# Optimization experiments

Measured on AMD Instinct MI355X. Metric: run time of the kernel, lower is better.

## Reference

```python
import jax, jax.numpy as jnp
import numpy as np

# ---- quantization scales (per-tensor, as produced by from_float calibration) ----
IN_SCALE = 0.05      # ForwardTokenizer: fp32 hidden -> int8
ALPHA_Q = 1e-4       # W8A8B8O8 requant multipliers (already include 1/sqrt(head_dim) for q)
ALPHA_K = 1e-4
ALPHA_V = 1e-4
QK_ALPHA = 1e-3      # BMM_S8T_S8N_F32T dequant scale (q_scale * k_scale)
PV_ALPHA = 1.0/127.0 # BMM_S8T_S8N_S8T requant scale ((1/127)*v_scale/out_scale)
OUT_ALPHA = 1e-4     # W8A8BFP32OFP32 dequant scale
NUM_HEADS = 32


def _quant_i8(x, scale):
    # simulate int8 quantization in fp32 (values are exact small integers)
    return jnp.clip(jnp.round(x / scale), -128.0, 127.0)


def _w8a8b8o8(x_i8, W_i8, b_i8, alpha):
    # int8 GEMM with int8 bias, requantized to int8: clamp(round(alpha*(x@W^T) + b))
    acc = jnp.einsum('btd,ed->bte', x_i8, W_i8)  # int32 accumulator in fp32
    return jnp.clip(jnp.round(alpha * acc + b_i8), -128.0, 127.0)


def setup_inputs() -> dict:
    key = jax.random.key(0)
    ks = jax.random.split(key, 10)
    B, T, D = 2, 2048, 2560
    hidden_states = jax.random.normal(ks[0], (B, T, D), dtype=jnp.float32)
    # causal additive mask, shape (B,1,T,T)
    neg = jnp.float32(-1e9)
    causal = jnp.where(jnp.tril(jnp.ones((T, T), dtype=bool)), 0.0, neg)
    attention_mask = jnp.broadcast_to(causal[None, None], (B, 1, T, T)).astype(jnp.float32)
    # int8-valued weights/biases stored as fp32 integers in [-127,127]
    def i8(k, shape):
        return jax.random.randint(k, shape, -127, 128).astype(jnp.float32)
    Wq = i8(ks[1], (D, D)); bq = i8(ks[2], (D,))
    Wk = i8(ks[3], (D, D)); bk = i8(ks[4], (D,))
    Wv = i8(ks[5], (D, D)); bv = i8(ks[6], (D,))
    Wo = i8(ks[7], (D, D))
    bo = jax.random.normal(ks[8], (D,), dtype=jnp.float32) * 0.01  # fp32 out bias
    return {"hidden_states": hidden_states, "attention_mask": attention_mask,
            "Wq": Wq, "bq": bq, "Wk": Wk, "bk": bk, "Wv": Wv, "bv": bv,
            "Wo": Wo, "bo": bo}


def reference(hidden_states, attention_mask, Wq, bq, Wk, bk, Wv, bv, Wo, bo):
    B, T, D = hidden_states.shape
    H = NUM_HEADS
    Dh = D // H
    # ForwardTokenizer: fp32 -> int8
    x_i8 = _quant_i8(hidden_states, IN_SCALE)
    # fused int8 q/k/v projections (W8A8B8O8Linear)
    q = _w8a8b8o8(x_i8, Wq, bq, ALPHA_Q)
    k = _w8a8b8o8(x_i8, Wk, bk, ALPHA_K)
    v = _w8a8b8o8(x_i8, Wv, bv, ALPHA_V)
    # (B,T,D) -> (B,H,T,Dh)
    def shape(t):
        return t.reshape(B, T, H, Dh).transpose(0, 2, 1, 3)
    q, k, v = shape(q), shape(k), shape(v)
    # BMM_S8T_S8N_F32T: int8 q @ k^T dequantized to fp32
    attn_weights = QK_ALPHA * jnp.einsum('bhqd,bhkd->bhqk', q, k)
    attn_weights = attn_weights + attention_mask  # (B,H,T,T)
    attn_weights = jnp.maximum(attn_weights, jnp.finfo(jnp.float32).min)
    attn_probs = jax.nn.softmax(attn_weights, axis=-1)
    # requantize probs to int8: mul_(127).round_()
    p_i8 = jnp.round(attn_probs * 127.0)
    # BMM_S8T_S8N_S8T: int8 p @ v requantized to int8
    attn_out = jnp.clip(jnp.round(PV_ALPHA * jnp.einsum('bhqk,bhkd->bhqd', p_i8, v)), -128.0, 127.0)
    # (B,H,T,Dh) -> (B,T,D)
    attn_out = attn_out.transpose(0, 2, 1, 3).reshape(B, T, D)
    # W8A8BFP32OFP32Linear: int8 GEMM, fp32 dequant + fp32 bias
    out = OUT_ALPHA * jnp.einsum('btd,ed->bte', attn_out, Wo) + bo
    return out
```

## Files before the change

kernel.cpp:

```cpp
#include <hip/hip_runtime.h>
#include <stdint.h>

typedef int v4i __attribute__((ext_vector_type(4)));

#define MFMA_I8(a,b,c) __builtin_amdgcn_mfma_i32_16x16x64_i8(a,b,c,0,0,0)

#define TD 2560
#define TT 2048
#define TB 2
#define TH 32
#define TDH 80
#define TDHP 128
#define TM 4096

#define LOG2E_MS 1.4426950408889634e-3f
#define MASKI (-(1<<30))
#define MAGICF 12582912.0f

__device__ __forceinline__ float clamp8f(float v){ return fminf(fmaxf(v, -128.0f), 127.0f); }
__device__ __forceinline__ float fexp2(float x){ return __builtin_amdgcn_exp2f(x); }

__device__ __forceinline__ void gl_lds16(const int8_t* g, int8_t* l){
  __builtin_amdgcn_global_load_lds(
      (const __attribute__((address_space(1))) void*)g,
      (__attribute__((address_space(3))) void*)l, 16, 0, 0);
}

__global__ void k_quant(const float* __restrict__ x, int8_t* __restrict__ y, int n4){
  int stride = gridDim.x * blockDim.x;
  for (int i = blockIdx.x*blockDim.x + threadIdx.x; i < n4; i += stride){
    float4 v = ((const float4*)x)[i];
    char4 o;
    o.x = (int8_t)clamp8f(rintf(__fdiv_rn(v.x, 0.05f)));
    o.y = (int8_t)clamp8f(rintf(__fdiv_rn(v.y, 0.05f)));
    o.z = (int8_t)clamp8f(rintf(__fdiv_rn(v.z, 0.05f)));
    o.w = (int8_t)clamp8f(rintf(__fdiv_rn(v.w, 0.05f)));
    ((char4*)y)[i] = o;
  }
}

__global__ void k_conv4(const float* __restrict__ w0, const float* __restrict__ w1,
                        const float* __restrict__ w2, const float* __restrict__ w3,
                        int8_t* __restrict__ y0, int8_t* __restrict__ y1,
                        int8_t* __restrict__ y2, int8_t* __restrict__ y3, int n4){
  const int z = blockIdx.y;
  const float* w = z == 0 ? w0 : (z == 1 ? w1 : (z == 2 ? w2 : w3));
  int8_t* y = z == 0 ? y0 : (z == 1 ? y1 : (z == 2 ? y2 : y3));
  int stride = gridDim.x * blockDim.x;
  for (int i = blockIdx.x*blockDim.x + threadIdx.x; i < n4; i += stride){
    float4 v = ((const float4*)w)[i];
    char4 o;
    o.x = (int8_t)(int)rintf(v.x);
    o.y = (int8_t)(int)rintf(v.y);
    o.z = (int8_t)(int)rintf(v.z);
    o.w = (int8_t)(int)rintf(v.w);
    ((char4*)y)[i] = o;
  }
}

#define GSTAGE(bufi, k0) do{                                        \
    gl_lds16(xa0 + (k0), &As[bufi][(wv*16)*64]);                    \
    gl_lds16(xa1 + (k0), &As[bufi][(64 + wv*16)*64]);               \
    gl_lds16(wb0 + (k0), &Bs[bufi][(wv*16)*64]);                    \
    gl_lds16(wb1 + (k0), &Bs[bufi][(64 + wv*16)*64]); }while(0)

#define GCOMP(bufi) do{                                             \
    v4i a[4], b[4];                                                 \
    _Pragma("unroll")                                               \
    for (int mi = 0; mi < 4; ++mi)                                  \
      a[mi] = *(const v4i*)&As[bufi][(wr*64 + mi*16 + llo)*64 + sca];\
    _Pragma("unroll")                                               \
    for (int ni = 0; ni < 4; ++ni)                                  \
      b[ni] = *(const v4i*)&Bs[bufi][(wc*64 + ni*16 + llo)*64 + sca];\
    _Pragma("unroll")                                               \
    for (int mi = 0; mi < 4; ++mi)                                  \
      _Pragma("unroll")                                             \
      for (int ni = 0; ni < 4; ++ni)                                \
        acc[mi][ni] = MFMA_I8(a[mi], b[ni], acc[mi][ni]); }while(0)

#define GKLOOP do{                                                  \
    GSTAGE(0, 0);                                                   \
    _Pragma("unroll 1")                                             \
    for (int p = 0; p < 20; ++p){                                   \
      GSTAGE(1, (2*p+1)*64);                                        \
      asm volatile("s_waitcnt vmcnt(4)" ::: "memory");              \
      __builtin_amdgcn_s_barrier();                                 \
      GCOMP(0);                                                     \
      __builtin_amdgcn_s_barrier();                                 \
      if (p < 19){                                                  \
        GSTAGE(0, (2*p+2)*64);                                      \
        asm volatile("s_waitcnt vmcnt(4)" ::: "memory");            \
      } else {                                                      \
        asm volatile("s_waitcnt vmcnt(0)" ::: "memory");            \
      }                                                             \
      __builtin_amdgcn_s_barrier();                                 \
      GCOMP(1);                                                     \
      __builtin_amdgcn_s_barrier();                                 \
    } }while(0)

__global__ __launch_bounds__(256, 4) void k_qkvg(const int8_t* __restrict__ x,
    const int8_t* __restrict__ w0_, const int8_t* __restrict__ w1_, const int8_t* __restrict__ w2_,
    const float* __restrict__ b0_, const float* __restrict__ b1_, const float* __restrict__ b2_,
    int8_t* __restrict__ dq, int8_t* __restrict__ dk, int8_t* __restrict__ dv)
{
  __shared__ __align__(16) int8_t As[2][128*64];
  __shared__ __align__(16) int8_t Bs[2][128*64];
  const int z = blockIdx.z;
  const int8_t* w = z == 0 ? w0_ : (z == 1 ? w1_ : w2_);
  const float* bias = z == 0 ? b0_ : (z == 1 ? b1_ : b2_);
  const int m0 = blockIdx.x * 128, n0 = blockIdx.y * 128;
  const int t = threadIdx.x;
  const int wv = t >> 6, l = t & 63, lhi = (l >> 4) & 3, llo = l & 15;
  const int wr = wv >> 1, wc = wv & 1;
  const int grow = l >> 2;
  const int gcol = ((l & 3) ^ ((l >> 3) & 3)) * 16;

  const int8_t* xa0 = x + (size_t)(m0 + wv*16 + grow)*TD + gcol;
  const int8_t* xa1 = x + (size_t)(m0 + 64 + wv*16 + grow)*TD + gcol;
  const int8_t* wb0 = w + (size_t)(n0 + wv*16 + grow)*TD + gcol;
  const int8_t* wb1 = w + (size_t)(n0 + 64 + wv*16 + grow)*TD + gcol;

  const int sca = (lhi ^ ((llo >> 1) & 3)) << 4;

  v4i acc[4][4] = {};
  GKLOOP;

  #pragma unroll
  for (int mi = 0; mi < 4; ++mi)
  #pragma unroll
  for (int ni = 0; ni < 4; ++ni)
  #pragma unroll
  for (int r = 0; r < 4; ++r){
    int rowg = m0 + wr*64 + mi*16 + lhi*4 + r;
    int colg = n0 + wc*64 + ni*16 + llo;
    float fv = __fadd_rn(__fmul_rn(1e-4f, (float)acc[mi][ni][r]), bias[colg]);
    int8_t q8 = (int8_t)clamp8f(rintf(fv));
    int bb = rowg >> 11, tl = rowg & 2047;
    int hh = colg / 80, dh = colg - hh*80;
    if (z == 0)      dq[((size_t)(bb*TH + hh)*TT + tl)*TDHP + dh] = q8;
    else if (z == 1) dk[((size_t)(bb*TH + hh)*TT + tl)*TDHP + dh] = q8;
    else             dv[((size_t)(bb*TH + hh)*TDH + dh)*TT + tl] = q8;
  }
}

__global__ __launch_bounds__(256, 4) void k_oproj128(const int8_t* __restrict__ x,
    const int8_t* __restrict__ w, const float* __restrict__ bo,
    float* __restrict__ out)
{
  __shared__ __align__(16) int8_t As[2][128*64];
  __shared__ __align__(16) int8_t Bs[2][128*64];
  const int m0 = blockIdx.x * 128, n0 = blockIdx.y * 128;
  const int t = threadIdx.x;
  const int wv = t >> 6, l = t & 63, lhi = (l >> 4) & 3, llo = l & 15;
  const int wr = wv >> 1, wc = wv & 1;
  const int grow = l >> 2;
  const int gcol = ((l & 3) ^ ((l >> 3) & 3)) * 16;

  const int8_t* xa0 = x + (size_t)(m0 + wv*16 + grow)*TD + gcol;
  const int8_t* xa1 = x + (size_t)(m0 + 64 + wv*16 + grow)*TD + gcol;
  const int8_t* wb0 = w + (size_t)(n0 + wv*16 + grow)*TD + gcol;
  const int8_t* wb1 = w + (size_t)(n0 + 64 + wv*16 + grow)*TD + gcol;

  const int sca = (lhi ^ ((llo >> 1) & 3)) << 4;

  v4i acc[4][4] = {};
  GKLOOP;

  #pragma unroll
  for (int mi = 0; mi < 4; ++mi)
  #pragma unroll
  for (int ni = 0; ni < 4; ++ni)
  #pragma unroll
  for (int r = 0; r < 4; ++r){
    int rowg = m0 + wr*64 + mi*16 + lhi*4 + r;
    int colg = n0 + wc*64 + ni*16 + llo;
    out[(size_t)rowg*TD + colg] =
        __fadd_rn(__fmul_rn(1e-4f, (float)acc[mi][ni][r]), bo[colg]);
  }
}

__global__ __launch_bounds__(256, 6) void k_attn6(const int8_t* __restrict__ qb_,
    const int8_t* __restrict__ kb_, const int8_t* __restrict__ vt_,
    int8_t* __restrict__ ao)
{
  __shared__ __align__(16) int8_t Ks[64*128];
  const int flat = blockIdx.x;
  const int g = flat & 7, ii = flat >> 3;
  const int qt = 31 - (ii >> 3);
  const int pair = g*8 + (ii & 7);
  const int h = pair & 31, b = pair >> 5;

  const int t = threadIdx.x, wv = t >> 6, l = t & 63, lhi = (l >> 4) & 3, llo = l & 15;
  const size_t bh = (size_t)(b*TH + h);
  const int8_t* qb = qb_ + bh*TT*TDHP;
  const int8_t* kb = kb_ + bh*TT*TDHP;
  const int8_t* vb = vt_ + bh*TDH*TT;

  const int qw0 = qt*64 + wv*16;
  const int qg = qw0 + llo;
  const int ktmax = qt + 1;

  int koff0[4], koff1[4];
  #pragma unroll
  for (int sub = 0; sub < 4; ++sub){
    const int row = sub*16 + llo, sw = row & 7;
    koff0[sub] = row*128 + (((lhi  ) ^ sw) << 4);
    koff1[sub] = row*128 + (((lhi+4) ^ sw) << 4);
  }

  v4i qa0 = *(const v4i*)(qb + (size_t)(qw0 + llo)*TDHP + lhi*16);
  v4i qa1 = {0,0,0,0};
  if (lhi == 0) qa1 = *(const v4i*)(qb + (size_t)(qw0 + llo)*TDHP + 64);

  const int srow = t >> 2, scp = (t & 3) * 2, ssw = srow & 7;
  const int8_t* kg = kb + (size_t)srow*TDHP + scp*16;
  int8_t* sdst0 = &Ks[srow*128 + (((scp  ) ^ ssw) << 4)];
  int8_t* sdst1 = &Ks[srow*128 + (((scp+1) ^ ssw) << 4)];

  int   M  = MASKI;
  float cm = __fmul_rn(LOG2E_MS, (float)MASKI);
  float ls = 0.0f;

  v4i pr0 = *(const v4i*)(kg);
  v4i pr1 = *(const v4i*)(kg + 16);
  *(v4i*)sdst0 = pr0; *(v4i*)sdst1 = pr1;
  for (int kt = 0; kt < ktmax; ++kt){
    if (kt + 1 < ktmax){
      pr0 = *(const v4i*)(kg + (size_t)(kt+1)*64*TDHP);
      pr1 = *(const v4i*)(kg + (size_t)(kt+1)*64*TDHP + 16);
    }
    __syncthreads();
    int sv[4][4];
    if (kt < qt){
      #pragma unroll
      for (int sub = 0; sub < 4; ++sub){
        v4i kf0 = *(const v4i*)&Ks[koff0[sub]];
        v4i kf1 = *(const v4i*)&Ks[koff1[sub]];
        v4i d = {}; d = MFMA_I8(kf0, qa0, d); d = MFMA_I8(kf1, qa1, d);
        sv[sub][0]=d[0]; sv[sub][1]=d[1]; sv[sub][2]=d[2]; sv[sub][3]=d[3];
      }
    } else {
      #pragma unroll
      for (int sub = 0; sub < 4; ++sub){
        if (sub <= wv){
          v4i kf0 = *(const v4i*)&Ks[koff0[sub]];
          v4i kf1 = *(const v4i*)&Ks[koff1[sub]];
          v4i d = {}; d = MFMA_I8(kf0, qa0, d); d = MFMA_I8(kf1, qa1, d);
          const int base = kt*64 + sub*16 + lhi*4;
          #pragma unroll
          for (int r = 0; r < 4; ++r)
            sv[sub][r] = (base + r <= qg) ? d[r] : MASKI;
        } else {
          #pragma unroll
          for (int r = 0; r < 4; ++r) sv[sub][r] = MASKI;
        }
      }
    }
    int m0 = max(max(sv[0][0], sv[0][1]), sv[0][2]);
    int m1 = max(max(sv[0][3], sv[1][0]), sv[1][1]);
    int m2 = max(max(sv[1][2], sv[1][3]), sv[2][0]);
    int m3 = max(max(sv[2][1], sv[2][2]), sv[2][3]);
    int m4 = max(max(sv[3][0], sv[3][1]), sv[3][2]);
    int tm = max(max(max(m0, m1), max(m2, m3)), max(m4, sv[3][3]));
    int Mn = max(M, tm);
    float cmN = __fmul_rn(LOG2E_MS, (float)Mn);
    float fac = fexp2(__fsub_rn(cm, cmN));
    float tot = 0.0f;
    #pragma unroll
    for (int sub = 0; sub < 4; ++sub){
      float e0 = fexp2(__fmaf_rn((float)sv[sub][0], LOG2E_MS, -cmN));
      float e1 = fexp2(__fmaf_rn((float)sv[sub][1], LOG2E_MS, -cmN));
      float e2 = fexp2(__fmaf_rn((float)sv[sub][2], LOG2E_MS, -cmN));
      float e3 = fexp2(__fmaf_rn((float)sv[sub][3], LOG2E_MS, -cmN));
      tot = __fadd_rn(tot, __fadd_rn(__fadd_rn(e0, e1), __fadd_rn(e2, e3)));
    }
    ls = __fmaf_rn(ls, fac, tot);
    M = Mn; cm = cmN;
    __syncthreads();
    if (kt + 1 < ktmax){ *(v4i*)sdst0 = pr0; *(v4i*)sdst1 = pr1; }
  }

  float rq;
  {
    float mm = cm, ll = ls;
    #pragma unroll
    for (int off = 16; off < 64; off <<= 1){
      float om = __shfl_xor(mm, off);
      float ol = __shfl_xor(ll, off);
      float mn = fmaxf(mm, om);
      ll = __fadd_rn(__fmul_rn(ll, fexp2(__fsub_rn(mm, mn))),
                     __fmul_rn(ol, fexp2(__fsub_rn(om, mn))));
      mm = mn;
    }
    cm = mm;
    rq = __fdiv_rn(127.0f, ll);
  }

  v4i pacc[5] = {};
  pr0 = *(const v4i*)(kg);
  pr1 = *(const v4i*)(kg + 16);
  __syncthreads();
  *(v4i*)sdst0 = pr0; *(v4i*)sdst1 = pr1;
  for (int kt = 0; kt < ktmax; ++kt){
    if (kt + 1 < ktmax){
      pr0 = *(const v4i*)(kg + (size_t)(kt+1)*64*TDHP);
      pr1 = *(const v4i*)(kg + (size_t)(kt+1)*64*TDHP + 16);
    }
    __syncthreads();
    uint32_t w[4] = {0u,0u,0u,0u};
    if (kt < qt){
      #pragma unroll
      for (int sub = 0; sub < 4; ++sub){
        v4i kf0 = *(const v4i*)&Ks[koff0[sub]];
        v4i kf1 = *(const v4i*)&Ks[koff1[sub]];
        v4i d = {}; d = MFMA_I8(kf0, qa0, d); d = MFMA_I8(kf1, qa1, d);
        uint32_t u0 = __float_as_uint(__fmaf_rn(fexp2(__fmaf_rn((float)d[0], LOG2E_MS, -cm)), rq, MAGICF));
        uint32_t u1 = __float_as_uint(__fmaf_rn(fexp2(__fmaf_rn((float)d[1], LOG2E_MS, -cm)), rq, MAGICF));
        uint32_t u2 = __float_as_uint(__fmaf_rn(fexp2(__fmaf_rn((float)d[2], LOG2E_MS, -cm)), rq, MAGICF));
        uint32_t u3 = __float_as_uint(__fmaf_rn(fexp2(__fmaf_rn((float)d[3], LOG2E_MS, -cm)), rq, MAGICF));
        w[sub] = (u0 & 0xffu) | ((u1 & 0xffu) << 8) | ((u2 & 0xffu) << 16) | (u3 << 24);
      }
    } else {
      #pragma unroll
      for (int sub = 0; sub < 4; ++sub){
        if (sub <= wv){
          v4i kf0 = *(const v4i*)&Ks[koff0[sub]];
          v4i kf1 = *(const v4i*)&Ks[koff1[sub]];
          v4i d = {}; d = MFMA_I8(kf0, qa0, d); d = MFMA_I8(kf1, qa1, d);
          const int base = kt*64 + sub*16 + lhi*4;
          uint32_t wrd = 0u;
          #pragma unroll
          for (int r = 0; r < 4; ++r){
            int sel = (base + r <= qg) ? d[r] : MASKI;
            uint32_t u = __float_as_uint(__fmaf_rn(fexp2(__fmaf_rn((float)sel, LOG2E_MS, -cm)), rq, MAGICF));
            wrd |= (u & 0xffu) << (8*r);
          }
          w[sub] = wrd;
        }
      }
    }
    #pragma unroll
    for (int bb = 0; bb < 2; ++bb){
      const int dist = 16 << bb;
      const int gb = (lhi >> bb) & 1;
      uint32_t nw[4];
      #pragma unroll
      for (int s = 0; s < 4; ++s){
        uint32_t tv = __shfl_xor(w[s ^ (1 << bb)], dist);
        nw[s] = (((s >> bb) & 1) == gb) ? w[s] : tv;
      }
      w[0]=nw[0]; w[1]=nw[1]; w[2]=nw[2]; w[3]=nw[3];
    }
    v4i pa;
    pa[0]=(int)w[0]; pa[1]=(int)w[1]; pa[2]=(int)w[2]; pa[3]=(int)w[3];
    #pragma unroll
    for (int dt = 0; dt < 5; ++dt){
      v4i vf = *(const v4i*)(vb + (size_t)(dt*16 + llo)*TT + kt*64 + lhi*16);
      pacc[dt] = MFMA_I8(vf, pa, pacc[dt]);
    }
    __syncthreads();
    if (kt + 1 < ktmax){ *(v4i*)sdst0 = pr0; *(v4i*)sdst1 = pr1; }
  }

  #pragma unroll
  for (int dt = 0; dt < 5; ++dt){
    uint32_t ob = 0u;
    #pragma unroll
    for (int r = 0; r < 4; ++r){
      int vq = (int)clamp8f(rintf(__fmul_rn((float)pacc[dt][r], (float)(1.0/127.0))));
      ob |= ((uint32_t)(uint8_t)(int8_t)vq) << (8*r);
    }
    *(uint32_t*)(ao + ((size_t)(b*TT) + qw0 + llo)*TD + h*TDH + dt*16 + lhi*4) = ob;
  }
}

extern "C" void kernel_launch(void* const* d_in, const int* in_sizes, int n_in,
                              void* d_out, int out_size, void* d_ws, size_t ws_size,
                              hipStream_t stream) {
  const float* hidden = (const float*)d_in[0];
  const float* Wq = (const float*)d_in[2];
  const float* bq = (const float*)d_in[3];
  const float* Wk = (const float*)d_in[4];
  const float* bk = (const float*)d_in[5];
  const float* Wv = (const float*)d_in[6];
  const float* bv = (const float*)d_in[7];
  const float* Wo = (const float*)d_in[8];
  const float* bo = (const float*)d_in[9];
  float* out = (float*)d_out;

  char* ws = (char*)d_ws;
  const size_t SZ_X  = (size_t)TM * TD;
  const size_t SZ_W  = (size_t)TD * TD;
  const size_t SZ_QK = (size_t)TB * TH * TT * TDHP;
  const size_t SZ_V  = (size_t)TB * TH * TDH * TT;
  int8_t* x8   = (int8_t*)ws;
  int8_t* wq8  = (int8_t*)(ws + SZ_X);
  int8_t* wk8  = wq8 + SZ_W;
  int8_t* wv8  = wk8 + SZ_W;
  int8_t* wo8  = wv8 + SZ_W;
  int8_t* qpad = wo8 + SZ_W;
  int8_t* kpad = qpad + SZ_QK;
  int8_t* vt   = kpad + SZ_QK;
  int8_t* ao   = vt + SZ_V;

  k_quant<<<4096, 256, 0, stream>>>(hidden, x8, (int)(SZ_X/4));
  k_conv4<<<dim3(1024, 4), 256, 0, stream>>>(Wq, Wk, Wv, Wo, wq8, wk8, wv8, wo8, (int)(SZ_W/4));

  k_qkvg<<<dim3(TM/128, TD/128, 3), 256, 0, stream>>>(x8, wq8, wk8, wv8, bq, bk, bv,
                                                      qpad, kpad, vt);

  k_attn6<<<dim3(2048), 256, 0, stream>>>(qpad, kpad, vt, ao);

  k_oproj128<<<dim3(TM/128, TD/128), 256, 0, stream>>>(ao, wo8, bo, out);
}
```

Measured before the change: 307.3 us.

## Load GEMM fragments directly from global memory into registers, dropping LDS staging

The QKV and output-projection GEMM kernels no longer stage tiles through shared memory with global_load_lds and barriers. Each lane now loads its MFMA operand fragments straight from global memory into registers, double-buffered across two k-steps, and the launch bounds are removed. This removes LDS traffic and barrier synchronization. In exchange, data shared between waves is no longer reused through LDS, so global and L2 traffic roughly doubles, and each lane reads 16-byte chunks from strided rows, which coalesces poorly.

```diff
diff --git a/kernel.cpp b/kernel.cpp
--- a/kernel.cpp
+++ b/kernel.cpp
@@ -58,53 +58,36 @@
   }
 }
 
-#define GSTAGE(bufi, k0) do{                                        \
-    gl_lds16(xa0 + (k0), &As[bufi][(wv*16)*64]);                    \
-    gl_lds16(xa1 + (k0), &As[bufi][(64 + wv*16)*64]);               \
-    gl_lds16(wb0 + (k0), &Bs[bufi][(wv*16)*64]);                    \
-    gl_lds16(wb1 + (k0), &Bs[bufi][(64 + wv*16)*64]); }while(0)
-
-#define GCOMP(bufi) do{                                             \
-    v4i a[4], b[4];                                                 \
+#define DRLOAD(ar, br, k0) do{                                      \
     _Pragma("unroll")                                               \
     for (int mi = 0; mi < 4; ++mi)                                  \
-      a[mi] = *(const v4i*)&As[bufi][(wr*64 + mi*16 + llo)*64 + sca];\
+      ar[mi] = *(const v4i*)(apx + (size_t)mi*16*TD + (k0));        \
     _Pragma("unroll")                                               \
     for (int ni = 0; ni < 4; ++ni)                                  \
-      b[ni] = *(const v4i*)&Bs[bufi][(wc*64 + ni*16 + llo)*64 + sca];\
+      br[ni] = *(const v4i*)(bpx + (size_t)ni*16*TD + (k0)); }while(0)
+
+#define DRMFMA(ar, br) do{                                          \
     _Pragma("unroll")                                               \
     for (int mi = 0; mi < 4; ++mi)                                  \
       _Pragma("unroll")                                             \
       for (int ni = 0; ni < 4; ++ni)                                \
-        acc[mi][ni] = MFMA_I8(a[mi], b[ni], acc[mi][ni]); }while(0)
-
-#define GKLOOP do{                                                  \
-    GSTAGE(0, 0);                                                   \
+        acc[mi][ni] = MFMA_I8(ar[mi], br[ni], acc[mi][ni]); }while(0)
+
+#define DRKLOOP do{                                                 \
+    DRLOAD(fa0, fb0, 0);                                            \
     _Pragma("unroll 1")                                             \
     for (int p = 0; p < 20; ++p){                                   \
-      GSTAGE(1, (2*p+1)*64);                                        \
-      asm volatile("s_waitcnt vmcnt(4)" ::: "memory");              \
-      __builtin_amdgcn_s_barrier();                                 \
-      GCOMP(0);                                                     \
-      __builtin_amdgcn_s_barrier();                                 \
-      if (p < 19){                                                  \
-        GSTAGE(0, (2*p+2)*64);                                      \
-        asm volatile("s_waitcnt vmcnt(4)" ::: "memory");            \
-      } else {                                                      \
-        asm volatile("s_waitcnt vmcnt(0)" ::: "memory");            \
-      }                                                             \
-      __builtin_amdgcn_s_barrier();                                 \
-      GCOMP(1);                                                     \
-      __builtin_amdgcn_s_barrier();                                 \
+      DRLOAD(fa1, fb1, (2*p+1)*64);                                 \
+      DRMFMA(fa0, fb0);                                             \
+      if (p < 19) DRLOAD(fa0, fb0, (2*p+2)*64);                     \
+      DRMFMA(fa1, fb1);                                             \
     } }while(0)
 
-__global__ __launch_bounds__(256, 4) void k_qkvg(const int8_t* __restrict__ x,
+__global__ void k_qkvg(const int8_t* __restrict__ x,
     const int8_t* __restrict__ w0_, const int8_t* __restrict__ w1_, const int8_t* __restrict__ w2_,
     const float* __restrict__ b0_, const float* __restrict__ b1_, const float* __restrict__ b2_,
     int8_t* __restrict__ dq, int8_t* __restrict__ dk, int8_t* __restrict__ dv)
 {
-  __shared__ __align__(16) int8_t As[2][128*64];
-  __shared__ __align__(16) int8_t Bs[2][128*64];
   const int z = blockIdx.z;
   const int8_t* w = z == 0 ? w0_ : (z == 1 ? w1_ : w2_);
   const float* bias = z == 0 ? b0_ : (z == 1 ? b1_ : b2_);
@@ -112,18 +95,13 @@
   const int t = threadIdx.x;
   const int wv = t >> 6, l = t & 63, lhi = (l >> 4) & 3, llo = l & 15;
   const int wr = wv >> 1, wc = wv & 1;
-  const int grow = l >> 2;
-  const int gcol = ((l & 3) ^ ((l >> 3) & 3)) * 16;
-
-  const int8_t* xa0 = x + (size_t)(m0 + wv*16 + grow)*TD + gcol;
-  const int8_t* xa1 = x + (size_t)(m0 + 64 + wv*16 + grow)*TD + gcol;
-  const int8_t* wb0 = w + (size_t)(n0 + wv*16 + grow)*TD + gcol;
-  const int8_t* wb1 = w + (size_t)(n0 + 64 + wv*16 + grow)*TD + gcol;
-
-  const int sca = (lhi ^ ((llo >> 1) & 3)) << 4;
+
+  const int8_t* apx = x + (size_t)(m0 + wr*64 + llo)*TD + lhi*16;
+  const int8_t* bpx = w + (size_t)(n0 + wc*64 + llo)*TD + lhi*16;
 
   v4i acc[4][4] = {};
-  GKLOOP;
+  v4i fa0[4], fb0[4], fa1[4], fb1[4];
+  DRKLOOP;
 
   #pragma unroll
   for (int mi = 0; mi < 4; ++mi)
@@ -143,28 +121,21 @@
   }
 }
 
-__global__ __launch_bounds__(256, 4) void k_oproj128(const int8_t* __restrict__ x,
+__global__ void k_oproj128(const int8_t* __restrict__ x,
     const int8_t* __restrict__ w, const float* __restrict__ bo,
     float* __restrict__ out)
 {
-  __shared__ __align__(16) int8_t As[2][128*64];
-  __shared__ __align__(16) int8_t Bs[2][128*64];
   const int m0 = blockIdx.x * 128, n0 = blockIdx.y * 128;
   const int t = threadIdx.x;
   const int wv = t >> 6, l = t & 63, lhi = (l >> 4) & 3, llo = l & 15;
   const int wr = wv >> 1, wc = wv & 1;
-  const int grow = l >> 2;
-  const int gcol = ((l & 3) ^ ((l >> 3) & 3)) * 16;
-
-  const int8_t* xa0 = x + (size_t)(m0 + wv*16 + grow)*TD + gcol;
-  const int8_t* xa1 = x + (size_t)(m0 + 64 + wv*16 + grow)*TD + gcol;
-  const int8_t* wb0 = w + (size_t)(n0 + wv*16 + grow)*TD + gcol;
-  const int8_t* wb1 = w + (size_t)(n0 + 64 + wv*16 + grow)*TD + gcol;
-
-  const int sca = (lhi ^ ((llo >> 1) & 3)) << 4;
+
+  const int8_t* apx = x + (size_t)(m0 + wr*64 + llo)*TD + lhi*16;
+  const int8_t* bpx = w + (size_t)(n0 + wc*64 + llo)*TD + lhi*16;
 
   v4i acc[4][4] = {};
-  GKLOOP;
+  v4i fa0[4], fb0[4], fa1[4], fb1[4];
+  DRKLOOP;
 
   #pragma unroll
   for (int mi = 0; mi < 4; ++mi)
```

Result: slower. 561.3 us (+82.7%).
